# Performance work log

Measured on AMD Instinct MI355X. Metric: run time of the kernel, lower is better.

## Reference

```python
import jax, jax.numpy as jnp
import numpy as np

B, T, D = 32, 512, 512
MAX_DUR = 8               # durations drawn from [0, MAX_DUR)
MAX_FRAMES = T * (MAX_DUR - 1)  # 3584 -> static upper bound on expanded length; pad to it
MAX_FRAMES = 4096          # round up to a nice static size


def setup_inputs() -> dict:
    key = jax.random.key(0)
    kx, kd = jax.random.split(key)
    x = jax.random.normal(kx, (B, T, D), dtype=jnp.float32)
    durations = jax.random.randint(kd, (B, T), 0, MAX_DUR, dtype=jnp.int32)
    return {"x": x, "durations": durations}


def reference(x, durations):
    # x: [B, T, D] float, durations: [B, T] int
    # Expansion via cumsum offsets + searchsorted gather (fused equivalent of
    # the host loop of repeat/cat/pad in the torch module).
    ends = jnp.cumsum(durations, axis=1)          # [B, T] exclusive end offsets
    total = ends[:, -1]                            # [B] true expanded lengths
    pos = jnp.arange(MAX_FRAMES, dtype=ends.dtype) # [F]
    # frame p belongs to token t where starts[t] <= p < ends[t]
    idx = jax.vmap(lambda e: jnp.searchsorted(e, pos, side='right'))(ends)  # [B, F]
    idx = jnp.clip(idx, 0, x.shape[1] - 1)
    out = jnp.take_along_axis(x, idx[:, :, None], axis=1)  # [B, F, D]
    mask = pos[None, :] < total[:, None]                    # [B, F]
    out = out * mask[:, :, None].astype(out.dtype)          # zero-pad beyond mel_len
    # torch fallback: an all-zero-duration row yields one zero frame, len 1
    mel_lens = jnp.maximum(total, 1).astype(jnp.int32)
    return out, mel_lens
```

## Files before the change

kernel.cpp:

```cpp
#include <hip/hip_runtime.h>
#include <hip/hip_bf16.h>

#define B_ 32
#define T_ 512
#define D_ 512
#define MAXF_ 4096

__global__ __launch_bounds__(512) void lr_scan_kernel(const int* __restrict__ dur,
                                                      int* __restrict__ ends,
                                                      float* __restrict__ mel_out) {
    __shared__ int s[T_];
    const int b = blockIdx.x;
    const int t = threadIdx.x;
    s[t] = dur[b * T_ + t];
    __syncthreads();
    #pragma unroll
    for (int off = 1; off < T_; off <<= 1) {
        int tmp = (t >= off) ? s[t - off] : 0;
        __syncthreads();
        s[t] += tmp;
        __syncthreads();
    }
    ends[b * T_ + t] = s[t];
    if (t == T_ - 1) {
        int total = s[T_ - 1];
        mel_out[b] = (float)(total > 1 ? total : 1);
    }
}

__global__ __launch_bounds__(256) void lr_gather_kernel(const float* __restrict__ x,
                                                        const int* __restrict__ ends,
                                                        float* __restrict__ out) {
    __shared__ int s_ends[T_];
    const int b = blockIdx.y;
    const int* eb = ends + b * T_;
    for (int i = threadIdx.y * 128 + threadIdx.x; i < T_; i += 256)
        s_ends[i] = eb[i];
    __syncthreads();

    const int total = s_ends[T_ - 1];
    const int p = blockIdx.x * 2 + threadIdx.y;
    const int tx = threadIdx.x;

    float4* orow = (float4*)(out + ((size_t)b * MAXF_ + p) * D_);
    if (p >= total) {
        orow[tx] = make_float4(0.f, 0.f, 0.f, 0.f);
    } else {
        int lo = 0, hi = T_;
        while (lo < hi) {
            int mid = (lo + hi) >> 1;
            if (s_ends[mid] <= p) lo = mid + 1;
            else hi = mid;
        }
        int idx = lo < (T_ - 1) ? lo : (T_ - 1);
        const float4* xrow = (const float4*)(x + ((size_t)b * T_ + idx) * D_);
        orow[tx] = xrow[tx];
    }
}

extern "C" void kernel_launch(void* const* d_in, const int* in_sizes, int n_in,
                              void* d_out, int out_size, void* d_ws, size_t ws_size,
                              hipStream_t stream) {
    const float* x = (const float*)d_in[0];
    const int* durations = (const int*)d_in[1];
    float* out = (float*)d_out;
    float* mel_out = out + (size_t)B_ * MAXF_ * D_;
    int* ends = (int*)d_ws;

    lr_scan_kernel<<<B_, T_, 0, stream>>>(durations, ends, mel_out);

    dim3 grid(MAXF_ / 2, B_);
    dim3 block(128, 2);
    lr_gather_kernel<<<grid, block, 0, stream>>>(x, ends, out);
}
```

Baseline: 308.8 us.

## Precompute per-frame source index map in scan kernel, simplify gather

The scan kernel now performs the binary search for every output frame and writes a frame-to-token index map (with -1 for padding frames), so the gather kernel no longer loads ends into shared memory or searches per block. The gather becomes a flat 1D float4 copy that reads one index per frame. This removes the per-block shared-memory load, the barrier and the redundant search from the 65536 gather blocks. In exchange the scan kernel does more serial work on only 32 blocks and writes a 512 KB index map.

```diff
diff --git a/kernel.cpp b/kernel.cpp
--- a/kernel.cpp
+++ b/kernel.cpp
@@ -6,9 +6,9 @@
 #define D_ 512
 #define MAXF_ 4096
 
-__global__ __launch_bounds__(512) void lr_scan_kernel(const int* __restrict__ dur,
-                                                      int* __restrict__ ends,
-                                                      float* __restrict__ mel_out) {
+__global__ __launch_bounds__(512) void lr_scan_idx_kernel(const int* __restrict__ dur,
+                                                          int* __restrict__ idx_map,
+                                                          float* __restrict__ mel_out) {
     __shared__ int s[T_];
     const int b = blockIdx.x;
     const int t = threadIdx.x;
@@ -21,41 +21,40 @@
         s[t] += tmp;
         __syncthreads();
     }
-    ends[b * T_ + t] = s[t];
+    const int total = s[T_ - 1];
     if (t == T_ - 1) {
-        int total = s[T_ - 1];
         mel_out[b] = (float)(total > 1 ? total : 1);
+    }
+    for (int p = t; p < MAXF_; p += T_) {
+        int v = -1;
+        if (p < total) {
+            int lo = 0, hi = T_;
+            while (lo < hi) {
+                int mid = (lo + hi) >> 1;
+                if (s[mid] <= p) lo = mid + 1;
+                else hi = mid;
+            }
+            v = lo < (T_ - 1) ? lo : (T_ - 1);
+        }
+        idx_map[b * MAXF_ + p] = v;
     }
 }
 
-__global__ __launch_bounds__(256) void lr_gather_kernel(const float* __restrict__ x,
-                                                        const int* __restrict__ ends,
-                                                        float* __restrict__ out) {
-    __shared__ int s_ends[T_];
-    const int b = blockIdx.y;
-    const int* eb = ends + b * T_;
-    for (int i = threadIdx.y * 128 + threadIdx.x; i < T_; i += 256)
-        s_ends[i] = eb[i];
-    __syncthreads();
-
-    const int total = s_ends[T_ - 1];
-    const int p = blockIdx.x * 2 + threadIdx.y;
-    const int tx = threadIdx.x;
-
-    float4* orow = (float4*)(out + ((size_t)b * MAXF_ + p) * D_);
-    if (p >= total) {
-        orow[tx] = make_float4(0.f, 0.f, 0.f, 0.f);
+__global__ __launch_bounds__(256) void lr_gather_kernel(const float4* __restrict__ x,
+                                                        const int* __restrict__ idx_map,
+                                                        float4* __restrict__ out) {
+    const size_t gid = (size_t)blockIdx.x * 256 + threadIdx.x;
+    const int frame = (int)(gid >> 7);
+    const int c = (int)(gid & 127);
+    const int idx = idx_map[frame];
+    float4 v;
+    if (idx < 0) {
+        v = make_float4(0.f, 0.f, 0.f, 0.f);
     } else {
-        int lo = 0, hi = T_;
-        while (lo < hi) {
-            int mid = (lo + hi) >> 1;
-            if (s_ends[mid] <= p) lo = mid + 1;
-            else hi = mid;
-        }
-        int idx = lo < (T_ - 1) ? lo : (T_ - 1);
-        const float4* xrow = (const float4*)(x + ((size_t)b * T_ + idx) * D_);
-        orow[tx] = xrow[tx];
+        const int b = frame >> 12;
+        v = x[((size_t)(b * T_ + idx) << 7) + c];
     }
+    out[gid] = v;
 }
 
 extern "C" void kernel_launch(void* const* d_in, const int* in_sizes, int n_in,
@@ -65,11 +64,11 @@
     const int* durations = (const int*)d_in[1];
     float* out = (float*)d_out;
     float* mel_out = out + (size_t)B_ * MAXF_ * D_;
-    int* ends = (int*)d_ws;
+    int* idx_map = (int*)d_ws;
 
-    lr_scan_kernel<<<B_, T_, 0, stream>>>(durations, ends, mel_out);
+    lr_scan_idx_kernel<<<B_, T_, 0, stream>>>(durations, idx_map, mel_out);
 
-    dim3 grid(MAXF_ / 2, B_);
-    dim3 block(128, 2);
-    lr_gather_kernel<<<grid, block, 0, stream>>>(x, ends, out);
+    const size_t n_vec4 = (size_t)B_ * MAXF_ * (D_ / 4);
+    lr_gather_kernel<<<(int)(n_vec4 / 256), 256, 0, stream>>>(
+        (const float4*)x, idx_map, (float4*)out);
 }
```

Measured after the change: 306.4 us. No clear change (-0.8%).
